# Kernel tuning notes

Hardware: AMD Instinct MI355X
Metric: run time of the kernel (lower is better)

Reference implementation:

```python
import jax, jax.numpy as jnp
import numpy as np

COMMITMENT_COST = 0.25
NUM_EMBEDDINGS = 8192
EMBEDDING_DIM = 256


def setup_inputs() -> dict:
    key = jax.random.key(0)
    k1, k2 = jax.random.split(key)
    inputs = jax.random.normal(k1, (32, 256, EMBEDDING_DIM), dtype=jnp.float32)
    codebook = jax.random.normal(k2, (NUM_EMBEDDINGS, EMBEDDING_DIM), dtype=jnp.float32)
    # match nn.Embedding init: N(0,1) then L2-normalize rows
    codebook = codebook / jnp.linalg.norm(codebook, axis=1, keepdims=True)
    return {"inputs": inputs, "codebook": codebook}


def reference(inputs, codebook):
    B, K, D = inputs.shape
    flat = inputs.reshape(-1, D).astype(jnp.float32)  # [N, D], N = B*K
    N = flat.shape[0]

    distances = (
        jnp.sum(flat * flat, axis=1, keepdims=True)
        + jnp.sum(codebook * codebook, axis=1)
        - 2.0 * flat @ codebook.T
    )
    indices = jnp.argmin(distances, axis=1)  # [N]

    # codebook lookup (equivalent to one-hot @ codebook)
    quantized = codebook[indices].reshape(B, K, D)

    e_latent_loss = jnp.mean((jax.lax.stop_gradient(quantized) - inputs) ** 2)
    q_latent_loss = jnp.mean((quantized - jax.lax.stop_gradient(inputs)) ** 2)
    loss = q_latent_loss + COMMITMENT_COST * e_latent_loss

    # straight-through estimator
    quantized_ste = inputs + jax.lax.stop_gradient(quantized - inputs)

    # perplexity from codebook usage histogram (== mean of one-hot encodings)
    counts = jnp.zeros((NUM_EMBEDDINGS,), dtype=jnp.float32).at[indices].add(1.0)
    avg_probs = counts / N
    perplexity = jnp.exp(-jnp.sum(avg_probs * jnp.log(avg_probs + 1e-10)))

    return quantized_ste, loss, perplexity
```

## Files before the change

kernel.cpp:

```cpp
#include <hip/hip_runtime.h>
#include <math.h>

#define NTOK 8192
#define NEMB 8192
#define DIM  256

typedef _Float16 f16x8 __attribute__((ext_vector_type(8)));
typedef _Float16 f16x4 __attribute__((ext_vector_type(4)));
typedef float    f32x4 __attribute__((ext_vector_type(4)));

__global__ __launch_bounds__(256) void convert_kernel(
        const float* __restrict__ X, const float* __restrict__ C,
        _Float16* __restrict__ Xh, _Float16* __restrict__ Ch,
        float* __restrict__ cnorm, float* __restrict__ xnorm,
        unsigned long long* __restrict__ keys, int* __restrict__ aux_zero) {
    const bool isC = (blockIdx.y != 0);
    if (isC && blockIdx.x < 8) {
        ((int4*)aux_zero)[blockIdx.x * 256 + threadIdx.x] = make_int4(0, 0, 0, 0);
    }
    if (!isC && blockIdx.x < 8) {
        int4 ff = make_int4(-1, -1, -1, -1);
        ((int4*)keys)[blockIdx.x * 512 + threadIdx.x * 2]     = ff;
        ((int4*)keys)[blockIdx.x * 512 + threadIdx.x * 2 + 1] = ff;
    }
    const float* src = isC ? C : X;
    _Float16* dst = isC ? Ch : Xh;
    size_t t = (size_t)blockIdx.x * 256 + threadIdx.x;
    float4 x = *(const float4*)&src[t * 4];
    f16x4 h;
    h[0] = (_Float16)x.x; h[1] = (_Float16)x.y;
    h[2] = (_Float16)x.z; h[3] = (_Float16)x.w;
    *(f16x4*)&dst[t * 4] = h;
    float s = x.x * x.x + x.y * x.y + x.z * x.z + x.w * x.w;
    #pragma unroll
    for (int off = 32; off >= 1; off >>= 1) s += __shfl_xor(s, off);
    if ((threadIdx.x & 63) == 0) {
        if (isC) cnorm[t >> 6] = s; else xnorm[t >> 6] = s;
    }
}

__device__ __forceinline__ void stage_pair(
        const _Float16* __restrict__ Ag, const _Float16* __restrict__ Bg,
        _Float16* Abase, _Float16* Bbase, int t) {
    #pragma unroll
    for (int c = 0; c < 4; ++c) {
        int gr  = c * 256 + t;
        int row = gr >> 3;
        int kg  = (gr & 7) ^ (row & 7);
        __builtin_amdgcn_global_load_lds(
            (const __attribute__((address_space(1))) void*)(Ag + (size_t)row * DIM + kg * 8),
            (__attribute__((address_space(3))) void*)(Abase + (size_t)gr * 8), 16, 0, 0);
        __builtin_amdgcn_global_load_lds(
            (const __attribute__((address_space(1))) void*)(Bg + (size_t)row * DIM + kg * 8),
            (__attribute__((address_space(3))) void*)(Bbase + (size_t)gr * 8), 16, 0, 0);
    }
}

__device__ __forceinline__ void compute_pair(
        const _Float16* Abase, const _Float16* Bbase,
        f32x4 (&acc)[4][4], int wm, int wn, int lrow, int g) {
    #pragma unroll
    for (int ks = 0; ks < 2; ++ks) {
        const int kg = ks * 4 + g;
        f16x8 af[4], bf_[4];
        #pragma unroll
        for (int tm = 0; tm < 4; ++tm) {
            int row = wm + tm * 16 + lrow;
            af[tm] = *(const f16x8*)&Abase[(row * 8 + (kg ^ (row & 7))) * 8];
        }
        #pragma unroll
        for (int tn = 0; tn < 4; ++tn) {
            int row = wn + tn * 16 + lrow;
            bf_[tn] = *(const f16x8*)&Bbase[(row * 8 + (kg ^ (row & 7))) * 8];
        }
        #pragma unroll
        for (int tm = 0; tm < 4; ++tm)
            #pragma unroll
            for (int tn = 0; tn < 4; ++tn)
                acc[tm][tn] = __builtin_amdgcn_mfma_f32_16x16x32_f16(
                    af[tm], bf_[tn], acc[tm][tn], 0, 0, 0);
    }
}

__global__ __launch_bounds__(256) void mfma_argmin_kernel(
        const _Float16* __restrict__ Xh, const _Float16* __restrict__ Ch,
        const float* __restrict__ cnorm,
        unsigned long long* __restrict__ keys) {
    __shared__ __align__(16) _Float16 lds[32768];

    const int t = threadIdx.x;
    const int wid = t >> 6, lane = t & 63;
    const int tb0 = blockIdx.x * 128;
    const int cb0 = blockIdx.y * 128;
    const int wm = (wid >> 1) * 64;
    const int wn = (wid & 1) * 64;
    const int lrow = lane & 15;
    const int g = lane >> 4;

    f32x4 acc[4][4];
    #pragma unroll
    for (int a = 0; a < 4; ++a)
        #pragma unroll
        for (int b = 0; b < 4; ++b) acc[a][b] = (f32x4)0.0f;

    const _Float16* Ag = Ch + (size_t)cb0 * DIM;
    const _Float16* Bg = Xh + (size_t)tb0 * DIM;

    stage_pair(Ag, Bg, lds, lds + 8192, t);
    __syncthreads();
    #pragma unroll
    for (int p = 0; p < 4; ++p) {
        _Float16* cur = lds + (p & 1) * 16384;
        if (p < 3) {
            _Float16* nxt = lds + ((p + 1) & 1) * 16384;
            stage_pair(Ag + (p + 1) * 64, Bg + (p + 1) * 64, nxt, nxt + 8192, t);
        }
        compute_pair(cur, cur + 8192, acc, wm, wn, lrow, g);
        __syncthreads();
    }

    float* cn_lds = (float*)lds;
    float* cmb_v  = (float*)lds + 128;
    int*   cmb_i  = (int*)((float*)lds + 384);
    if (t < 128) cn_lds[t] = cnorm[cb0 + t];
    __syncthreads();

    float cn[16];
    #pragma unroll
    for (int tm = 0; tm < 4; ++tm)
        #pragma unroll
        for (int reg = 0; reg < 4; ++reg)
            cn[tm * 4 + reg] = cn_lds[wm + tm * 16 + g * 4 + reg];

    #pragma unroll
    for (int tn = 0; tn < 4; ++tn) {
        float bv = 1e30f; int bi = 0x7fffffff;
        #pragma unroll
        for (int tm = 0; tm < 4; ++tm) {
            #pragma unroll
            for (int reg = 0; reg < 4; ++reg) {
                float d = fmaf(-2.0f, acc[tm][tn][reg], cn[tm * 4 + reg]);
                int code = cb0 + wm + tm * 16 + g * 4 + reg;
                if (d < bv) { bv = d; bi = code; }
            }
        }
        #pragma unroll
        for (int off = 16; off <= 32; off <<= 1) {
            float ov = __shfl_xor(bv, off);
            int   oi = __shfl_xor(bi, off);
            if (ov < bv || (ov == bv && oi < bi)) { bv = ov; bi = oi; }
        }
        if (g == 0) {
            int tl = wn + tn * 16 + lrow;
            cmb_v[tl * 2 + (wid >> 1)] = bv;
            cmb_i[tl * 2 + (wid >> 1)] = bi;
        }
    }
    __syncthreads();
    if (t < 128) {
        float v0 = cmb_v[t * 2], v1 = cmb_v[t * 2 + 1];
        int   i0 = cmb_i[t * 2], i1 = cmb_i[t * 2 + 1];
        bool tk = (v1 < v0) || (v1 == v0 && i1 < i0);
        float bv = tk ? v1 : v0;
        int   bi = tk ? i1 : i0;
        unsigned long long key =
            ((unsigned long long)__builtin_bit_cast(unsigned, bv + 64.0f) << 32)
            | (unsigned)bi;
        atomicMin(&keys[tb0 + t], key);
    }
}

__global__ __launch_bounds__(256) void gather_kernel(
        const float* __restrict__ C, const unsigned long long* __restrict__ keys,
        const float* __restrict__ xnorm, int* __restrict__ counts,
        float* __restrict__ out, float* __restrict__ psum) {
    __shared__ int idx_lds[32];
    const int m0 = blockIdx.x * 32;
    const int t = threadIdx.x;
    if (t < 32) {
        unsigned long long k = keys[m0 + t];
        int bi  = (int)(unsigned)k;
        float d = __builtin_bit_cast(float, (unsigned)(k >> 32)) - 64.0f;
        idx_lds[t] = bi;
        atomicAdd(&counts[bi], 1);
        float lt = d + xnorm[m0 + t];
        #pragma unroll
        for (int off = 1; off < 32; off <<= 1) lt += __shfl_xor(lt, off);
        if (t == 0) psum[blockIdx.x] = lt;
    }
    __syncthreads();
    const int wid = t >> 6, lane = t & 63;
    #pragma unroll
    for (int r = 0; r < 8; ++r) {
        int token = m0 + wid * 8 + r;
        int e = idx_lds[wid * 8 + r];
        float4 q = *(const float4*)&C[(size_t)e * DIM + lane * 4];
        *(float4*)&out[(size_t)token * DIM + lane * 4] = q;
    }
}

__global__ __launch_bounds__(256) void finalize_kernel(
        const int* __restrict__ counts, const float* __restrict__ psum,
        float* __restrict__ out) {
    const int t = threadIdx.x;
    double local = 0.0;
    #pragma unroll 1
    for (int e = t; e < NEMB; e += 256) {
        float p = (float)counts[e] * (1.0f / (float)NTOK);
        local += (double)(p * logf(p + 1e-10f));
    }
    float ls = psum[t];
    #pragma unroll
    for (int off = 32; off >= 1; off >>= 1) {
        local += __shfl_xor(local, off);
        ls    += __shfl_xor(ls, off);
    }
    __shared__ double she[4];
    __shared__ float  shs[4];
    int lane = t & 63, wid = t >> 6;
    if (lane == 0) { she[wid] = local; shs[wid] = ls; }
    __syncthreads();
    if (t == 0) {
        double ent = she[0] + she[1] + she[2] + she[3];
        float  ssq = shs[0] + shs[1] + shs[2] + shs[3];
        out[(size_t)NTOK * DIM]     = 1.25f * ssq / (float)((size_t)NTOK * DIM);
        out[(size_t)NTOK * DIM + 1] = expf((float)(-ent));
    }
}

extern "C" void kernel_launch(void* const* d_in, const int* in_sizes, int n_in,
                              void* d_out, int out_size, void* d_ws, size_t ws_size,
                              hipStream_t stream) {
    const float* X = (const float*)d_in[0];
    const float* C = (const float*)d_in[1];
    float* out = (float*)d_out;

    char* ws = (char*)d_ws;
    size_t o = 0;
    _Float16* Xh = (_Float16*)(ws + o); o += (size_t)NTOK * DIM * 2;
    _Float16* Ch = (_Float16*)(ws + o); o += (size_t)NEMB * DIM * 2;
    float* cnorm = (float*)(ws + o); o += (size_t)NEMB * 4;
    float* xnorm = (float*)(ws + o); o += (size_t)NTOK * 4;
    unsigned long long* keys = (unsigned long long*)(ws + o); o += (size_t)NTOK * 8;
    int* counts  = (int*)(ws + o);   o += (size_t)NEMB * 4;
    float* psum  = (float*)(ws + o);

    convert_kernel<<<dim3(NTOK * DIM / 4 / 256, 2), 256, 0, stream>>>(
        X, C, Xh, Ch, cnorm, xnorm, keys, counts);
    mfma_argmin_kernel<<<dim3(NTOK / 128, NEMB / 128), 256, 0, stream>>>(
        Xh, Ch, cnorm, keys);
    gather_kernel<<<256, 256, 0, stream>>>(
        C, keys, xnorm, counts, out, psum);
    finalize_kernel<<<1, 256, 0, stream>>>(counts, psum, out);
}
```

Before: 139.1 us.

## Fuse gather into argmin kernel via last-block-done counter per token tile

Removes the separate gather kernel. Each argmin block bumps a per-token-tile completion counter, and the last of the 64 codebook-tile blocks for that token tile reads the final keys through an atomic. That block then does the codebook gather, the histogram counts and the per-tile loss partial sums. This saves one kernel launch and its tail. In exchange, 64 blocks do the gather with only 256 threads each, serially at the end of the grid, and the pattern relies on atomic visibility ordering across blocks.

```diff
diff --git a/kernel.cpp b/kernel.cpp
--- a/kernel.cpp
+++ b/kernel.cpp
@@ -13,11 +13,13 @@
         const float* __restrict__ X, const float* __restrict__ C,
         _Float16* __restrict__ Xh, _Float16* __restrict__ Ch,
         float* __restrict__ cnorm, float* __restrict__ xnorm,
-        unsigned long long* __restrict__ keys, int* __restrict__ aux_zero) {
+        unsigned long long* __restrict__ keys, int* __restrict__ counts,
+        int* __restrict__ done) {
     const bool isC = (blockIdx.y != 0);
     if (isC && blockIdx.x < 8) {
-        ((int4*)aux_zero)[blockIdx.x * 256 + threadIdx.x] = make_int4(0, 0, 0, 0);
-    }
+        ((int4*)counts)[blockIdx.x * 256 + threadIdx.x] = make_int4(0, 0, 0, 0);
+    }
+    if (isC && blockIdx.x == 8 && threadIdx.x < 64) done[threadIdx.x] = 0;
     if (!isC && blockIdx.x < 8) {
         int4 ff = make_int4(-1, -1, -1, -1);
         ((int4*)keys)[blockIdx.x * 512 + threadIdx.x * 2]     = ff;
@@ -84,9 +86,12 @@
 
 __global__ __launch_bounds__(256) void mfma_argmin_kernel(
         const _Float16* __restrict__ Xh, const _Float16* __restrict__ Ch,
-        const float* __restrict__ cnorm,
-        unsigned long long* __restrict__ keys) {
+        const float* __restrict__ cnorm, unsigned long long* __restrict__ keys,
+        const float* __restrict__ C, const float* __restrict__ xnorm,
+        int* __restrict__ counts, float* __restrict__ out,
+        float* __restrict__ psum, int* __restrict__ done) {
     __shared__ __align__(16) _Float16 lds[32768];
+    __shared__ int last;
 
     const int t = threadIdx.x;
     const int wid = t >> 6, lane = t & 63;
@@ -168,32 +173,31 @@
             | (unsigned)bi;
         atomicMin(&keys[tb0 + t], key);
     }
-}
-
-__global__ __launch_bounds__(256) void gather_kernel(
-        const float* __restrict__ C, const unsigned long long* __restrict__ keys,
-        const float* __restrict__ xnorm, int* __restrict__ counts,
-        float* __restrict__ out, float* __restrict__ psum) {
-    __shared__ int idx_lds[32];
-    const int m0 = blockIdx.x * 32;
-    const int t = threadIdx.x;
-    if (t < 32) {
-        unsigned long long k = keys[m0 + t];
+
+    __syncthreads();
+    if (t == 0) last = (atomicAdd(&done[blockIdx.x], 1) == 63);
+    __syncthreads();
+    if (!last) return;
+
+    int*   idx_lds = (int*)lds;
+    float* wsum    = (float*)((char*)lds + 512);
+    if (t < 128) {
+        unsigned long long k = atomicMin(&keys[tb0 + t], ~0ull);
         int bi  = (int)(unsigned)k;
         float d = __builtin_bit_cast(float, (unsigned)(k >> 32)) - 64.0f;
         idx_lds[t] = bi;
         atomicAdd(&counts[bi], 1);
-        float lt = d + xnorm[m0 + t];
-        #pragma unroll
-        for (int off = 1; off < 32; off <<= 1) lt += __shfl_xor(lt, off);
-        if (t == 0) psum[blockIdx.x] = lt;
-    }
-    __syncthreads();
-    const int wid = t >> 6, lane = t & 63;
-    #pragma unroll
-    for (int r = 0; r < 8; ++r) {
-        int token = m0 + wid * 8 + r;
-        int e = idx_lds[wid * 8 + r];
+        float lt = d + xnorm[tb0 + t];
+        #pragma unroll
+        for (int off = 32; off >= 1; off >>= 1) lt += __shfl_xor(lt, off);
+        if (lane == 0) wsum[wid] = lt;
+    }
+    __syncthreads();
+    if (t == 0) psum[blockIdx.x] = wsum[0] + wsum[1];
+    #pragma unroll 1
+    for (int r = 0; r < 32; ++r) {
+        int token = tb0 + wid * 32 + r;
+        int e = idx_lds[wid * 32 + r];
         float4 q = *(const float4*)&C[(size_t)e * DIM + lane * 4];
         *(float4*)&out[(size_t)token * DIM + lane * 4] = q;
     }
@@ -209,7 +213,7 @@
         float p = (float)counts[e] * (1.0f / (float)NTOK);
         local += (double)(p * logf(p + 1e-10f));
     }
-    float ls = psum[t];
+    float ls = (t < 64) ? psum[t] : 0.0f;
     #pragma unroll
     for (int off = 32; off >= 1; off >>= 1) {
         local += __shfl_xor(local, off);
@@ -243,13 +247,12 @@
     float* xnorm = (float*)(ws + o); o += (size_t)NTOK * 4;
     unsigned long long* keys = (unsigned long long*)(ws + o); o += (size_t)NTOK * 8;
     int* counts  = (int*)(ws + o);   o += (size_t)NEMB * 4;
+    int* done    = (int*)(ws + o);   o += 64 * 4;
     float* psum  = (float*)(ws + o);
 
     convert_kernel<<<dim3(NTOK * DIM / 4 / 256, 2), 256, 0, stream>>>(
-        X, C, Xh, Ch, cnorm, xnorm, keys, counts);
+        X, C, Xh, Ch, cnorm, xnorm, keys, counts, done);
     mfma_argmin_kernel<<<dim3(NTOK / 128, NEMB / 128), 256, 0, stream>>>(
-        Xh, Ch, cnorm, keys);
-    gather_kernel<<<256, 256, 0, stream>>>(
-        C, keys, xnorm, counts, out, psum);
+        Xh, Ch, cnorm, keys, C, xnorm, counts, out, psum, done);
     finalize_kernel<<<1, 256, 0, stream>>>(counts, psum, out);
 }
```

After: 151.8 us. 9.1% more time.
